# Optimization experiments

Hardware: AMD Instinct MI355X
Metric: run time of the kernel (lower is better)

The kernel has to match this reference:

```python
import jax, jax.numpy as jnp
import numpy as np

DIM = 512
HEADS = 8
HEAD_DIM = DIM // HEADS
B, N = 2, 16 * 14 * 14  # input_size=(16,14,14) -> N=3136
SCALE = HEAD_DIM ** -0.5


def setup_inputs() -> dict:
    key = jax.random.key(0)
    kx, kq, kk, kv, kp = jax.random.split(key, 5)
    s = DIM ** -0.5  # keep pre-softmax logits reasonable
    return {
        "x": jax.random.normal(kx, (B, N, DIM), dtype=jnp.float32),
        "wq": jax.random.normal(kq, (DIM, DIM), dtype=jnp.float32) * s,
        "wk": jax.random.normal(kk, (DIM, DIM), dtype=jnp.float32) * s,
        "wv": jax.random.normal(kv, (DIM, DIM), dtype=jnp.float32) * s,
        "wproj": jax.random.normal(kp, (DIM, DIM), dtype=jnp.float32) * s,
    }


def reference(x, wq, wk, wv, wproj):
    Bs, Ns, C = x.shape
    # nn.Linear computes x @ W.T; split heads -> [B, H, N, hd]
    def heads(y):
        return y.reshape(Bs, Ns, HEADS, HEAD_DIM).transpose(0, 2, 1, 3)
    q = heads(x @ wq.T)
    k = heads(x @ wk.T)
    v = heads(x @ wv.T)
    attn = jnp.einsum("bhnd,bhmd->bhnm", q, k) * SCALE  # [B,H,N,N]
    attn = jax.nn.softmax(attn, axis=-1)
    out = jnp.einsum("bhnm,bhmd->bhnd", attn, v)
    out = out.transpose(0, 2, 1, 3).reshape(Bs, Ns, C)
    return out @ wproj.T
```

## Files before the change

### kernel.cpp

```cpp
#include <hip/hip_runtime.h>
#include <hip/hip_bf16.h>
#include <stdint.h>

#define SEQ   3136
#define NDIM  512
#define NBH   16
#define QROWS 50176

typedef __bf16 bf16x8 __attribute__((ext_vector_type(8)));
typedef float  f32x4  __attribute__((ext_vector_type(4)));
typedef unsigned short u16;
typedef u16 u16x8 __attribute__((ext_vector_type(8)));
typedef u16 u16x4 __attribute__((ext_vector_type(4)));

__device__ __forceinline__ u16 bfr(float f) { return __builtin_bit_cast(u16, (__bf16)f); }
__device__ __forceinline__ int swzf(int row) { return (row & 3) | ((row >> 1) & 4); }
__device__ __forceinline__ f32x4 mfma16(bf16x8 a, bf16x8 b, f32x4 c) {
  return __builtin_amdgcn_mfma_f32_16x16x32_bf16(a, b, c, 0, 0, 0);
}
__device__ __forceinline__ bf16x8 lds_frag(const u16* base, int row, int logical) {
  return __builtin_bit_cast(bf16x8,
      *(const u16x8*)((const char*)base + row * 128 + (logical ^ (swzf(row) << 4))));
}
__device__ __forceinline__ void gload16(const void* g, void* l) {
  __builtin_amdgcn_global_load_lds((const __attribute__((address_space(1))) void*)g,
                                   (__attribute__((address_space(3))) void*)l, 16, 0, 0);
}

__device__ __forceinline__ void cvt8(const float* src, u16* dst) {
  const f32x4* p = (const f32x4*)src;
  f32x4 a = p[0], b = p[1];
  u16x8 o;
  o[0]=bfr(a[0]); o[1]=bfr(a[1]); o[2]=bfr(a[2]); o[3]=bfr(a[3]);
  o[4]=bfr(b[0]); o[5]=bfr(b[1]); o[6]=bfr(b[2]); o[7]=bfr(b[3]);
  *(u16x8*)dst = o;
}

extern "C" __global__ void cvt_x(const float* __restrict__ x, u16* __restrict__ xb) {
  int i = (blockIdx.x * 256 + threadIdx.x) * 8;
  cvt8(x + i, xb + i);
}
extern "C" __global__ void cvt_w(const float* __restrict__ wq, const float* __restrict__ wk,
                                 const float* __restrict__ wv, const float* __restrict__ wp,
                                 u16* __restrict__ wb, u16* __restrict__ wpb) {
  int y = blockIdx.y;
  const float* src = y == 0 ? wq : y == 1 ? wk : y == 2 ? wv : wp;
  u16* dst = y < 3 ? wb + (size_t)y * 262144 : wpb;
  int i = (blockIdx.x * 256 + threadIdx.x) * 8;
  cvt8(src + i, dst + i);
}

extern "C" __global__ __launch_bounds__(256, 2)
void qkv_kernel(const u16* __restrict__ xb, const u16* __restrict__ wb,
                u16* __restrict__ Qg, u16* __restrict__ Kg, u16* __restrict__ Vtg)
{
  __shared__ __align__(16) u16 smem[4 * 8192];
  const int tid = threadIdx.x, lane = tid & 63, wid = tid >> 6;
  const int g = lane >> 4, lr = lane & 15;
  const int wr = wid >> 1, wc = wid & 1;
  const int m0 = blockIdx.x * 128;
  const int f0 = blockIdx.y * 128;
  const int which = f0 >> 9;
  const int f0w = f0 & 511;

  f32x4 acc[4][4] = {};

  auto stage = [&](int buf, int k0) {
#pragma unroll
    for (int c = 0; c < 4; ++c) {
      int seg = wid * 4 + c;
      int row = seg * 8 + (lane >> 3);
      int lc = (lane & 7) ^ swzf(row);
      gload16(xb + (size_t)(m0 + row) * NDIM + k0 + lc * 8,
              smem + buf * 8192 + seg * 512);
      gload16(wb + (size_t)(f0 + row) * NDIM + k0 + lc * 8,
              smem + 16384 + buf * 8192 + seg * 512);
    }
  };
  auto compute = [&](int buf) {
    const u16* A  = smem + buf * 8192;
    const u16* Bl = smem + 16384 + buf * 8192;
#pragma unroll
    for (int ks = 0; ks < 2; ++ks) {
      bf16x8 af[4], bg[4];
#pragma unroll
      for (int t = 0; t < 4; ++t) af[t] = lds_frag(A,  wr * 64 + t * 16 + lr, ks * 64 + g * 16);
#pragma unroll
      for (int t = 0; t < 4; ++t) bg[t] = lds_frag(Bl, wc * 64 + t * 16 + lr, ks * 64 + g * 16);
#pragma unroll
      for (int tm = 0; tm < 4; ++tm)
#pragma unroll
        for (int tn = 0; tn < 4; ++tn)
          acc[tm][tn] = mfma16(af[tm], bg[tn], acc[tm][tn]);
    }
  };

  stage(0, 0);
  __syncthreads();
  int buf = 0;
#pragma unroll 1
  for (int k = 0; k < 8; ++k) {
    if (k < 7) stage(buf ^ 1, (k + 1) * 64);
    compute(buf);
    __syncthreads();
    buf ^= 1;
  }

  const float qscale = 0.18033688f;
  if (which < 2) {
    u16* Dst = which == 0 ? Qg : Kg;
    float sc = which == 0 ? qscale : 1.0f;
#pragma unroll
    for (int tm = 0; tm < 4; ++tm)
#pragma unroll
      for (int tn = 0; tn < 4; ++tn)
#pragma unroll
        for (int r = 0; r < 4; ++r) {
          int m = m0 + wr * 64 + tm * 16 + 4 * g + r;
          int b = m >= SEQ; int n = m - b * SEQ;
          int fm = f0w + wc * 64 + tn * 16 + lr;
          int h = fm >> 6, d = fm & 63;
          Dst[(((size_t)(b * 8 + h)) * SEQ + n) * 64 + d] = bfr(acc[tm][tn][r] * sc);
        }
  } else {
    u16* T = smem;
    __syncthreads();
#pragma unroll
    for (int tm = 0; tm < 4; ++tm)
#pragma unroll
      for (int tn = 0; tn < 4; ++tn) {
        int fl = wc * 64 + tn * 16 + lr;
        int t0 = wr * 64 + tm * 16 + 4 * g;
        u16x4 o;
        o[0]=bfr(acc[tm][tn][0]); o[1]=bfr(acc[tm][tn][1]);
        o[2]=bfr(acc[tm][tn][2]); o[3]=bfr(acc[tm][tn][3]);
        *(u16x4*)((char*)T + fl * 256 + ((t0 * 2) ^ ((fl & 7) << 4))) = o;
      }
    __syncthreads();
#pragma unroll
    for (int c = 0; c < 8; ++c) {
      int fl = tid >> 1, half = tid & 1;
      int tb = half * 128 + c * 16;
      u16x8 v = *(const u16x8*)((const char*)T + fl * 256 + (tb ^ ((fl & 7) << 4)));
      int fm = f0w + fl; int h = fm >> 6, d = fm & 63;
      int n0 = m0 + half * 64 + c * 8;
      int b = n0 >= SEQ; n0 -= b * SEQ;
      *(u16x8*)(Vtg + (((size_t)(b * 8 + h)) * 64 + d) * SEQ + n0) = v;
    }
  }
}

extern "C" __global__ __launch_bounds__(256)
void attn_kernel(const u16* __restrict__ Qg, const u16* __restrict__ Kg,
                 const u16* __restrict__ Vtg, float* __restrict__ Opart,
                 float2* __restrict__ mlb)
{
  __shared__ __align__(16) u16 smem[4 * 4096];
  const int tid = threadIdx.x, lane = tid & 63, wid = tid >> 6;
  const int g = lane >> 4, lr = lane & 15;
  const int q0 = blockIdx.x * 64;
  const int bh = blockIdx.y;
  const int split = blockIdx.z;
  const size_t bhN = (size_t)bh * SEQ;

  bf16x8 qf[2];
  {
    const u16* qp = Qg + (bhN + q0 + wid * 16 + lr) * 64;
    qf[0] = __builtin_bit_cast(bf16x8, *(const u16x8*)(qp + g * 8));
    qf[1] = __builtin_bit_cast(bf16x8, *(const u16x8*)(qp + 32 + g * 8));
  }

  f32x4 om[4] = {};
  f32x4 l_acc[4] = {};
  float m_run = -1e30f;

  auto stageT = [&](int buf, int t) {
    int kv0 = t * 64;
#pragma unroll
    for (int c = 0; c < 2; ++c) {
      int row = wid * 16 + c * 8 + (lane >> 3);
      int lc = (lane & 7) ^ swzf(row);
      gload16(Kg + (bhN + kv0 + row) * 64 + lc * 8,
              smem + buf * 8192 + (wid * 2 + c) * 512);
      gload16(Vtg + ((size_t)bh * 64 + row) * SEQ + kv0 + lc * 8,
              smem + 4096 + buf * 8192 + (wid * 2 + c) * 512);
    }
  };

  const int t0 = split * 25;
  const int nt = 25 - split;

  stageT(0, t0);
  __syncthreads();
  int buf = 0;
#pragma unroll 1
  for (int s = 0; s < nt; ++s) {
    if (s < nt - 1) stageT(buf ^ 1, t0 + s + 1);
    const u16* Kl = smem + buf * 8192;
    const u16* Vl = smem + 4096 + buf * 8192;

    f32x4 st[4] = {};
#pragma unroll
    for (int ks = 0; ks < 2; ++ks)
#pragma unroll
      for (int kt = 0; kt < 4; ++kt) {
        int row = (kt & 1) * 32 + (lr >> 2) * 8 + (kt >> 1) * 4 + (lr & 3);
        bf16x8 kf = lds_frag(Kl, row, ks * 64 + g * 16);
        st[kt] = mfma16(kf, qf[ks], st[kt]);
      }

    float tm = fmaxf(
        fmaxf(fmaxf(fmaxf(st[0][0], st[0][1]), fmaxf(st[0][2], st[0][3])),
              fmaxf(fmaxf(st[1][0], st[1][1]), fmaxf(st[1][2], st[1][3]))),
        fmaxf(fmaxf(fmaxf(st[2][0], st[2][1]), fmaxf(st[2][2], st[2][3])),
              fmaxf(fmaxf(st[3][0], st[3][1]), fmaxf(st[3][2], st[3][3]))));
    tm = fmaxf(tm, __shfl_xor(tm, 16));
    tm = fmaxf(tm, __shfl_xor(tm, 32));

    if (__any(tm > m_run + 8.0f)) {
      float mn = fmaxf(m_run, tm);
      float sc = exp2f(m_run - mn);
#pragma unroll
      for (int dt = 0; dt < 4; ++dt) om[dt] *= sc;
#pragma unroll
      for (int kt = 0; kt < 4; ++kt) l_acc[kt] *= sc;
      m_run = mn;
    }

    bf16x8 pa0, pa1;
#pragma unroll
    for (int kt = 0; kt < 4; ++kt)
#pragma unroll
      for (int r = 0; r < 4; ++r) {
        float p = exp2f(st[kt][r] - m_run);
        l_acc[kt][r] += p;
        if (kt & 1) pa1[(kt >> 1) * 4 + r] = (__bf16)p;
        else        pa0[(kt >> 1) * 4 + r] = (__bf16)p;
      }

#pragma unroll
    for (int dt = 0; dt < 4; ++dt) {
      bf16x8 v0 = lds_frag(Vl, dt * 16 + lr, g * 16);
      bf16x8 v1 = lds_frag(Vl, dt * 16 + lr, 64 + g * 16);
      om[dt] = mfma16(v0, pa0, om[dt]);
      om[dt] = mfma16(v1, pa1, om[dt]);
    }
    __syncthreads();
    buf ^= 1;
  }

  f32x4 ls = l_acc[0] + l_acc[1] + l_acc[2] + l_acc[3];
  float l_tot = ls[0] + ls[1] + ls[2] + ls[3];
  l_tot += __shfl_xor(l_tot, 16);
  l_tot += __shfl_xor(l_tot, 32);

  int n = q0 + wid * 16 + lr;
  float* Ob = Opart + ((size_t)(split * NBH + bh) * SEQ + n) * 64;
#pragma unroll
  for (int dt = 0; dt < 4; ++dt)
    *(f32x4*)(Ob + dt * 16 + 4 * g) = om[dt];
  if (g == 0)
    mlb[(size_t)split * QROWS + bhN + n] = make_float2(m_run, l_tot);
}

extern "C" __global__ void combine_kernel(const float* __restrict__ Opart,
                                          const float2* __restrict__ mlb,
                                          u16* __restrict__ Og)
{
  const int tid = threadIdx.x;
  const int n = blockIdx.x * 32 + (tid >> 3);
  const int bh = blockIdx.y;
  const int dc = (tid & 7) * 8;
  const size_t R = (size_t)bh * SEQ + n;

  float2 a = mlb[R], b = mlb[QROWS + R];
  float m = fmaxf(a.x, b.x);
  float w0 = exp2f(a.x - m), w1 = exp2f(b.x - m);
  float inv = 1.0f / (a.y * w0 + b.y * w1);
  w0 *= inv; w1 *= inv;

  const float* p0 = Opart + R * 64 + dc;
  const float* p1 = Opart + (size_t)QROWS * 64 + R * 64 + dc;
  f32x4 o0a = *(const f32x4*)p0, o0b = *(const f32x4*)(p0 + 4);
  f32x4 o1a = *(const f32x4*)p1, o1b = *(const f32x4*)(p1 + 4);
  u16x8 o;
#pragma unroll
  for (int j = 0; j < 4; ++j) {
    o[j]     = bfr(o0a[j] * w0 + o1a[j] * w1);
    o[4 + j] = bfr(o0b[j] * w0 + o1b[j] * w1);
  }
  *(u16x8*)(Og + ((size_t)(bh >> 3) * SEQ + n) * NDIM + (bh & 7) * 64 + dc) = o;
}

extern "C" __global__ __launch_bounds__(256, 2)
void proj_kernel(const u16* __restrict__ Og, const u16* __restrict__ wpb,
                 float* __restrict__ out)
{
  __shared__ __align__(16) u16 smem[4 * 4096];
  const int tid = threadIdx.x, lane = tid & 63, wid = tid >> 6;
  const int g = lane >> 4, lr = lane & 15;
  const int m0 = blockIdx.x * 64;
  const int f0 = blockIdx.y * 64;

  f32x4 acc[4] = {};

  auto stage = [&](int buf, int k0) {
#pragma unroll
    for (int c = 0; c < 2; ++c) {
      int seg = wid * 2 + c;
      int row = seg * 8 + (lane >> 3);
      int lc = (lane & 7) ^ swzf(row);
      gload16(Og + (size_t)(m0 + row) * NDIM + k0 + lc * 8,
              smem + buf * 4096 + seg * 512);
      gload16(wpb + (size_t)(f0 + row) * NDIM + k0 + lc * 8,
              smem + 8192 + buf * 4096 + seg * 512);
    }
  };
  auto compute = [&](int buf) {
    const u16* A  = smem + buf * 4096;
    const u16* Bl = smem + 8192 + buf * 4096;
#pragma unroll
    for (int ks = 0; ks < 2; ++ks) {
      bf16x8 af = lds_frag(A, wid * 16 + lr, ks * 64 + g * 16);
#pragma unroll
      for (int t = 0; t < 4; ++t) {
        bf16x8 bg = lds_frag(Bl, t * 16 + lr, ks * 64 + g * 16);
        acc[t] = mfma16(af, bg, acc[t]);
      }
    }
  };

  stage(0, 0);
  __syncthreads();
  int buf = 0;
#pragma unroll 1
  for (int k = 0; k < 8; ++k) {
    if (k < 7) stage(buf ^ 1, (k + 1) * 64);
    compute(buf);
    __syncthreads();
    buf ^= 1;
  }

#pragma unroll
  for (int t = 0; t < 4; ++t)
#pragma unroll
    for (int r = 0; r < 4; ++r) {
      int m = m0 + wid * 16 + 4 * g + r;
      out[(size_t)m * NDIM + f0 + t * 16 + lr] = acc[t][r];
    }
}

extern "C" void kernel_launch(void* const* d_in, const int* in_sizes, int n_in,
                              void* d_out, int out_size, void* d_ws, size_t ws_size,
                              hipStream_t stream) {
  const float* x     = (const float*)d_in[0];
  const float* wq    = (const float*)d_in[1];
  const float* wk    = (const float*)d_in[2];
  const float* wv    = (const float*)d_in[3];
  const float* wproj = (const float*)d_in[4];
  float* out = (float*)d_out;

  const size_t E = (size_t)QROWS * 64;
  u16*   xb    = (u16*)d_ws;
  u16*   wb    = xb + E;
  u16*   wpb   = wb + 1536 * 512;
  u16*   Qg    = wpb + 512 * 512;
  u16*   Kg    = Qg + E;
  u16*   Vtg   = Kg + E;
  float* Opart = (float*)(Vtg + E);
  float2* mlb  = (float2*)(Opart + 2 * E);
  u16*   Og    = xb;

  cvt_x         <<<dim3(1568),      256, 0, stream>>>(x, xb);
  cvt_w         <<<dim3(128, 4),    256, 0, stream>>>(wq, wk, wv, wproj, wb, wpb);
  qkv_kernel    <<<dim3(49, 12),    256, 0, stream>>>(xb, wb, Qg, Kg, Vtg);
  attn_kernel   <<<dim3(49, 16, 2), 256, 0, stream>>>(Qg, Kg, Vtg, Opart, mlb);
  combine_kernel<<<dim3(98, 16),    256, 0, stream>>>(Opart, mlb, Og);
  proj_kernel   <<<dim3(98, 8),     256, 0, stream>>>(Og, wpb, out);
}
```

Baseline: 203.3 us.

## Merge conversion kernels, widen QKV blocks, compute softmax row sums via MFMA

Fuses the x and weight fp32-to-bf16 conversions into one launch. The QKV GEMM moves to 512-thread blocks, with each wave owning a 32x64 tile. This halves per-wave accumulators and raises wave count per block. The attention kernel now computes the softmax denominator with an MFMA against a ones vector instead of per-element adds and a final reduction. It also hoists K/V address math into incremented pointers, defers the cross-lane max shuffle into the rare rescale branch, and wraps MFMA groups in s_setprio. The tradeoff is extra MFMA work for the row sums, plus more LDS contention from larger blocks.

```diff
diff --git a/kernel.cpp b/kernel.cpp
--- a/kernel.cpp
+++ b/kernel.cpp
@@ -6,6 +6,8 @@
 #define NDIM  512
 #define NBH   16
 #define QROWS 50176
+#define XE    3211264
+#define WE    262144
 
 typedef __bf16 bf16x8 __attribute__((ext_vector_type(8)));
 typedef float  f32x4  __attribute__((ext_vector_type(4)));
@@ -36,21 +38,22 @@
   *(u16x8*)dst = o;
 }
 
-extern "C" __global__ void cvt_x(const float* __restrict__ x, u16* __restrict__ xb) {
-  int i = (blockIdx.x * 256 + threadIdx.x) * 8;
-  cvt8(x + i, xb + i);
-}
-extern "C" __global__ void cvt_w(const float* __restrict__ wq, const float* __restrict__ wk,
-                                 const float* __restrict__ wv, const float* __restrict__ wp,
-                                 u16* __restrict__ wb, u16* __restrict__ wpb) {
-  int y = blockIdx.y;
-  const float* src = y == 0 ? wq : y == 1 ? wk : y == 2 ? wv : wp;
-  u16* dst = y < 3 ? wb + (size_t)y * 262144 : wpb;
-  int i = (blockIdx.x * 256 + threadIdx.x) * 8;
-  cvt8(src + i, dst + i);
-}
-
-extern "C" __global__ __launch_bounds__(256, 2)
+extern "C" __global__ void cvt_all(const float* __restrict__ x, const float* __restrict__ wq,
+                                   const float* __restrict__ wk, const float* __restrict__ wv,
+                                   const float* __restrict__ wp,
+                                   u16* __restrict__ xb, u16* __restrict__ wall) {
+  size_t gid = (size_t)(blockIdx.x * 256 + threadIdx.x) * 8;
+  if (gid < XE) {
+    cvt8(x + gid, xb + gid);
+  } else {
+    size_t j = gid - XE;
+    int which = (int)(j >> 18);
+    const float* s = which == 0 ? wq : which == 1 ? wk : which == 2 ? wv : wp;
+    cvt8(s + (j & (WE - 1)), wall + j);
+  }
+}
+
+extern "C" __global__ __launch_bounds__(512)
 void qkv_kernel(const u16* __restrict__ xb, const u16* __restrict__ wb,
                 u16* __restrict__ Qg, u16* __restrict__ Kg, u16* __restrict__ Vtg)
 {
@@ -63,18 +66,18 @@
   const int which = f0 >> 9;
   const int f0w = f0 & 511;
 
-  f32x4 acc[4][4] = {};
+  f32x4 acc[2][4] = {};
 
   auto stage = [&](int buf, int k0) {
 #pragma unroll
-    for (int c = 0; c < 4; ++c) {
-      int seg = wid * 4 + c;
-      int row = seg * 8 + (lane >> 3);
+    for (int c = 0; c < 2; ++c) {
+      int chunk = c * 512 + tid;
+      int row = chunk >> 3;
       int lc = (lane & 7) ^ swzf(row);
       gload16(xb + (size_t)(m0 + row) * NDIM + k0 + lc * 8,
-              smem + buf * 8192 + seg * 512);
+              smem + buf * 8192 + (c * 512 + wid * 64) * 8);
       gload16(wb + (size_t)(f0 + row) * NDIM + k0 + lc * 8,
-              smem + 16384 + buf * 8192 + seg * 512);
+              smem + 16384 + buf * 8192 + (c * 512 + wid * 64) * 8);
     }
   };
   auto compute = [&](int buf) {
@@ -82,16 +85,18 @@
     const u16* Bl = smem + 16384 + buf * 8192;
 #pragma unroll
     for (int ks = 0; ks < 2; ++ks) {
-      bf16x8 af[4], bg[4];
-#pragma unroll
-      for (int t = 0; t < 4; ++t) af[t] = lds_frag(A,  wr * 64 + t * 16 + lr, ks * 64 + g * 16);
+      bf16x8 af[2], bg[4];
+#pragma unroll
+      for (int t = 0; t < 2; ++t) af[t] = lds_frag(A,  wr * 32 + t * 16 + lr, ks * 64 + g * 16);
 #pragma unroll
       for (int t = 0; t < 4; ++t) bg[t] = lds_frag(Bl, wc * 64 + t * 16 + lr, ks * 64 + g * 16);
-#pragma unroll
-      for (int tm = 0; tm < 4; ++tm)
+      __builtin_amdgcn_s_setprio(1);
+#pragma unroll
+      for (int tm = 0; tm < 2; ++tm)
 #pragma unroll
         for (int tn = 0; tn < 4; ++tn)
           acc[tm][tn] = mfma16(af[tm], bg[tn], acc[tm][tn]);
+      __builtin_amdgcn_s_setprio(0);
     }
   };
 
@@ -111,12 +116,12 @@
     u16* Dst = which == 0 ? Qg : Kg;
     float sc = which == 0 ? qscale : 1.0f;
 #pragma unroll
-    for (int tm = 0; tm < 4; ++tm)
+    for (int tm = 0; tm < 2; ++tm)
 #pragma unroll
       for (int tn = 0; tn < 4; ++tn)
 #pragma unroll
         for (int r = 0; r < 4; ++r) {
-          int m = m0 + wr * 64 + tm * 16 + 4 * g + r;
+          int m = m0 + wr * 32 + tm * 16 + 4 * g + r;
           int b = m >= SEQ; int n = m - b * SEQ;
           int fm = f0w + wc * 64 + tn * 16 + lr;
           int h = fm >> 6, d = fm & 63;
@@ -124,26 +129,26 @@
         }
   } else {
     u16* T = smem;
-    __syncthreads();
-#pragma unroll
-    for (int tm = 0; tm < 4; ++tm)
+#pragma unroll
+    for (int tm = 0; tm < 2; ++tm)
 #pragma unroll
       for (int tn = 0; tn < 4; ++tn) {
         int fl = wc * 64 + tn * 16 + lr;
-        int t0 = wr * 64 + tm * 16 + 4 * g;
+        int t0r = wr * 32 + tm * 16 + 4 * g;
         u16x4 o;
         o[0]=bfr(acc[tm][tn][0]); o[1]=bfr(acc[tm][tn][1]);
         o[2]=bfr(acc[tm][tn][2]); o[3]=bfr(acc[tm][tn][3]);
-        *(u16x4*)((char*)T + fl * 256 + ((t0 * 2) ^ ((fl & 7) << 4))) = o;
+        *(u16x4*)((char*)T + fl * 256 + ((t0r * 2) ^ ((fl & 7) << 4))) = o;
       }
     __syncthreads();
 #pragma unroll
-    for (int c = 0; c < 8; ++c) {
-      int fl = tid >> 1, half = tid & 1;
-      int tb = half * 128 + c * 16;
+    for (int c = 0; c < 4; ++c) {
+      int chunk = c * 512 + tid;
+      int fl = chunk >> 4, tc = chunk & 15;
+      int tb = tc * 16;
       u16x8 v = *(const u16x8*)((const char*)T + fl * 256 + (tb ^ ((fl & 7) << 4)));
       int fm = f0w + fl; int h = fm >> 6, d = fm & 63;
-      int n0 = m0 + half * 64 + c * 8;
+      int n0 = m0 + tc * 8;
       int b = n0 >= SEQ; n0 -= b * SEQ;
       *(u16x8*)(Vtg + (((size_t)(b * 8 + h)) * 64 + d) * SEQ + n0) = v;
     }
@@ -169,61 +174,78 @@
     qf[0] = __builtin_bit_cast(bf16x8, *(const u16x8*)(qp + g * 8));
     qf[1] = __builtin_bit_cast(bf16x8, *(const u16x8*)(qp + 32 + g * 8));
   }
+  bf16x8 ones;
+  {
+    u16x8 ow; 
+#pragma unroll
+    for (int j = 0; j < 8; ++j) ow[j] = 0x3F80;
+    ones = __builtin_bit_cast(bf16x8, ow);
+  }
 
   f32x4 om[4] = {};
-  f32x4 l_acc[4] = {};
+  f32x4 lacc = {};
   float m_run = -1e30f;
 
-  auto stageT = [&](int buf, int t) {
-    int kv0 = t * 64;
-#pragma unroll
-    for (int c = 0; c < 2; ++c) {
-      int row = wid * 16 + c * 8 + (lane >> 3);
-      int lc = (lane & 7) ^ swzf(row);
-      gload16(Kg + (bhN + kv0 + row) * 64 + lc * 8,
-              smem + buf * 8192 + (wid * 2 + c) * 512);
-      gload16(Vtg + ((size_t)bh * 64 + row) * SEQ + kv0 + lc * 8,
-              smem + 4096 + buf * 8192 + (wid * 2 + c) * 512);
-    }
-  };
-
+  uint32_t koff[2], voff[2];
+#pragma unroll
+  for (int c = 0; c < 2; ++c) {
+    int row = wid * 16 + c * 8 + (lane >> 3);
+    int lc = (lane & 7) ^ swzf(row);
+    koff[c] = row * 64 + lc * 8;
+    voff[c] = row * SEQ + lc * 8;
+  }
   const int t0 = split * 25;
   const int nt = 25 - split;
-
-  stageT(0, t0);
+  const u16* kb = Kg + (bhN + t0 * 64) * 64;
+  const u16* vb = Vtg + (size_t)bh * (64 * SEQ) + t0 * 64;
+
+  auto stageT = [&](int buf, const u16* kp, const u16* vp) {
+#pragma unroll
+    for (int c = 0; c < 2; ++c) {
+      gload16(kp + koff[c], smem + buf * 8192 + (wid * 2 + c) * 512);
+      gload16(vp + voff[c], smem + 4096 + buf * 8192 + (wid * 2 + c) * 512);
+    }
+  };
+
+  stageT(0, kb, vb);
+  kb += 4096; vb += 64;
   __syncthreads();
   int buf = 0;
 #pragma unroll 1
   for (int s = 0; s < nt; ++s) {
-    if (s < nt - 1) stageT(buf ^ 1, t0 + s + 1);
+    if (s < nt - 1) { stageT(buf ^ 1, kb, vb); kb += 4096; vb += 64; }
     const u16* Kl = smem + buf * 8192;
     const u16* Vl = smem + 4096 + buf * 8192;
 
     f32x4 st[4] = {};
 #pragma unroll
-    for (int ks = 0; ks < 2; ++ks)
+    for (int ks = 0; ks < 2; ++ks) {
+      bf16x8 kf[4];
 #pragma unroll
       for (int kt = 0; kt < 4; ++kt) {
         int row = (kt & 1) * 32 + (lr >> 2) * 8 + (kt >> 1) * 4 + (lr & 3);
-        bf16x8 kf = lds_frag(Kl, row, ks * 64 + g * 16);
-        st[kt] = mfma16(kf, qf[ks], st[kt]);
+        kf[kt] = lds_frag(Kl, row, ks * 64 + g * 16);
       }
+      __builtin_amdgcn_s_setprio(1);
+#pragma unroll
+      for (int kt = 0; kt < 4; ++kt) st[kt] = mfma16(kf[kt], qf[ks], st[kt]);
+      __builtin_amdgcn_s_setprio(0);
+    }
 
     float tm = fmaxf(
         fmaxf(fmaxf(fmaxf(st[0][0], st[0][1]), fmaxf(st[0][2], st[0][3])),
               fmaxf(fmaxf(st[1][0], st[1][1]), fmaxf(st[1][2], st[1][3]))),
         fmaxf(fmaxf(fmaxf(st[2][0], st[2][1]), fmaxf(st[2][2], st[2][3])),
               fmaxf(fmaxf(st[3][0], st[3][1]), fmaxf(st[3][2], st[3][3]))));
-    tm = fmaxf(tm, __shfl_xor(tm, 16));
-    tm = fmaxf(tm, __shfl_xor(tm, 32));
 
     if (__any(tm > m_run + 8.0f)) {
-      float mn = fmaxf(m_run, tm);
+      float tmax = fmaxf(tm, __shfl_xor(tm, 16));
+      tmax = fmaxf(tmax, __shfl_xor(tmax, 32));
+      float mn = fmaxf(m_run, tmax);
       float sc = exp2f(m_run - mn);
 #pragma unroll
       for (int dt = 0; dt < 4; ++dt) om[dt] *= sc;
-#pragma unroll
-      for (int kt = 0; kt < 4; ++kt) l_acc[kt] *= sc;
+      lacc *= sc;
       m_run = mn;
     }
 
@@ -233,7 +255,6 @@
 #pragma unroll
       for (int r = 0; r < 4; ++r) {
         float p = exp2f(st[kt][r] - m_run);
-        l_acc[kt][r] += p;
         if (kt & 1) pa1[(kt >> 1) * 4 + r] = (__bf16)p;
         else        pa0[(kt >> 1) * 4 + r] = (__bf16)p;
       }
@@ -242,17 +263,16 @@
     for (int dt = 0; dt < 4; ++dt) {
       bf16x8 v0 = lds_frag(Vl, dt * 16 + lr, g * 16);
       bf16x8 v1 = lds_frag(Vl, dt * 16 + lr, 64 + g * 16);
+      __builtin_amdgcn_s_setprio(1);
       om[dt] = mfma16(v0, pa0, om[dt]);
       om[dt] = mfma16(v1, pa1, om[dt]);
-    }
+      __builtin_amdgcn_s_setprio(0);
+    }
+    lacc = mfma16(ones, pa0, lacc);
+    lacc = mfma16(ones, pa1, lacc);
     __syncthreads();
     buf ^= 1;
   }
-
-  f32x4 ls = l_acc[0] + l_acc[1] + l_acc[2] + l_acc[3];
-  float l_tot = ls[0] + ls[1] + ls[2] + ls[3];
-  l_tot += __shfl_xor(l_tot, 16);
-  l_tot += __shfl_xor(l_tot, 32);
 
   int n = q0 + wid * 16 + lr;
   float* Ob = Opart + ((size_t)(split * NBH + bh) * SEQ + n) * 64;
@@ -260,7 +280,7 @@
   for (int dt = 0; dt < 4; ++dt)
     *(f32x4*)(Ob + dt * 16 + 4 * g) = om[dt];
   if (g == 0)
-    mlb[(size_t)split * QROWS + bhN + n] = make_float2(m_run, l_tot);
+    mlb[(size_t)split * QROWS + bhN + n] = make_float2(m_run, lacc[0]);
 }
 
 extern "C" __global__ void combine_kernel(const float* __restrict__ Opart,
@@ -362,19 +382,17 @@
 
   const size_t E = (size_t)QROWS * 64;
   u16*   xb    = (u16*)d_ws;
-  u16*   wb    = xb + E;
-  u16*   wpb   = wb + 1536 * 512;
-  u16*   Qg    = wpb + 512 * 512;
+  u16*   wall  = xb + XE;
+  u16*   Qg    = wall + 4 * WE;
   u16*   Kg    = Qg + E;
   u16*   Vtg   = Kg + E;
   float* Opart = (float*)(Vtg + E);
   float2* mlb  = (float2*)(Opart + 2 * E);
   u16*   Og    = xb;
 
-  cvt_x         <<<dim3(1568),      256, 0, stream>>>(x, xb);
-  cvt_w         <<<dim3(128, 4),    256, 0, stream>>>(wq, wk, wv, wproj, wb, wpb);
-  qkv_kernel    <<<dim3(49, 12),    256, 0, stream>>>(xb, wb, Qg, Kg, Vtg);
+  cvt_all       <<<dim3(2080),      256, 0, stream>>>(x, wq, wk, wv, wproj, xb, wall);
+  qkv_kernel    <<<dim3(49, 12),    512, 0, stream>>>(xb, wall, Qg, Kg, Vtg);
   attn_kernel   <<<dim3(49, 16, 2), 256, 0, stream>>>(Qg, Kg, Vtg, Opart, mlb);
   combine_kernel<<<dim3(98, 16),    256, 0, stream>>>(Opart, mlb, Og);
-  proj_kernel   <<<dim3(98, 8),     256, 0, stream>>>(Og, wpb, out);
-}
+  proj_kernel   <<<dim3(98, 8),     256, 0, stream>>>(Og, wall + 3 * WE, out);
+}
```

Measured after the change: 190.5 us. 1.07x faster.
